# Kernel tuning notes

Hardware: AMD Instinct MI355X
Metric: run time of the kernel (lower is better)

The kernel has to match this reference:

```python
import jax, jax.numpy as jnp
import numpy as np

N, D, IN, HID, OUT, E = 20000, 8, 64, 128, 64, 100000
EPS = 1e-5


def _bn(h, g, b):
    # training-mode BatchNorm1d: biased batch variance, eps=1e-5
    m = h.mean(axis=0)
    v = jnp.mean((h - m) ** 2, axis=0)
    return (h - m) * jax.lax.rsqrt(v + EPS) * g + b


def setup_inputs() -> dict:
    key = jax.random.key(0)
    ks = jax.random.split(key, 12)
    x = jax.random.normal(ks[0], (N, IN), dtype=jnp.float32)
    node_ts = jax.random.uniform(ks[1], (N,), dtype=jnp.float32)
    neighbor_idx = jax.random.randint(ks[2], (N, D), 0, N, dtype=jnp.int32)
    neighbor_ts = jax.random.uniform(ks[3], (N, D), dtype=jnp.float32)
    target = jax.random.randint(ks[4], (2, E), 0, N, dtype=jnp.int32)
    neg_pairs = jax.random.randint(ks[5], (2, E), 0, N, dtype=jnp.int32)
    W1 = jax.random.normal(ks[6], (IN, HID), dtype=jnp.float32) * (1.0 / np.sqrt(IN))
    b1 = jnp.zeros((HID,), jnp.float32)
    g1 = jnp.ones((HID,), jnp.float32)
    be1 = jnp.zeros((HID,), jnp.float32)
    W2 = jax.random.normal(ks[7], (HID, OUT), dtype=jnp.float32) * (1.0 / np.sqrt(HID))
    b2 = jnp.zeros((OUT,), jnp.float32)
    g2 = jnp.ones((OUT,), jnp.float32)
    be2 = jnp.zeros((OUT,), jnp.float32)
    Wd = jax.random.normal(ks[8], (OUT, 1), dtype=jnp.float32) * (1.0 / np.sqrt(OUT))
    bd = jnp.zeros((1,), jnp.float32)
    return {"x": x, "node_ts": node_ts, "neighbor_idx": neighbor_idx,
            "neighbor_ts": neighbor_ts, "target": target, "neg_pairs": neg_pairs,
            "W1": W1, "b1": b1, "g1": g1, "be1": be1,
            "W2": W2, "b2": b2, "g2": g2, "be2": be2, "Wd": Wd, "bd": bd}


def reference(x, node_ts, neighbor_idx, neighbor_ts, target, neg_pairs,
              W1, b1, g1, be1, W2, b2, g2, be2, Wd, bd):
    n = jnp.arange(N, dtype=neighbor_idx.dtype)
    # ---- level-2 queries: every node at its own timestamp ----
    # children = D temporal-neighbor slots + self (self always valid, ts=node_ts)
    c_idx = jnp.concatenate([neighbor_idx, n[:, None]], axis=1)          # [N, D+1]
    c_ts = jnp.concatenate([neighbor_ts, node_ts[:, None]], axis=1)      # [N, D+1]
    mask2 = jnp.concatenate([neighbor_ts <= node_ts[:, None],
                             jnp.ones((N, 1), bool)], axis=1)            # [N, D+1]
    # ---- level-1 queries: each (child node, child ts) pair ----
    ci = c_idx.reshape(-1)                                               # [M]
    cts = c_ts.reshape(-1)
    gc_idx = jnp.concatenate([neighbor_idx[ci], ci[:, None]], axis=1)    # [M, D+1]
    mask1 = jnp.concatenate([neighbor_ts[ci] <= cts[:, None],
                             jnp.ones((ci.shape[0], 1), bool)], axis=1)
    # ---- layer 0: raw features of grandchildren ----
    h0 = x[gc_idx]                                                       # [M, D+1, IN]
    m1 = mask1.astype(x.dtype)
    agg1 = jnp.einsum('mk,mkf->mf', m1, h0) / m1.sum(1, keepdims=True)   # masked mean
    h1 = jax.nn.relu(_bn(agg1 @ W1 + b1, g1, be1))                       # [M, HID]
    h1 = h1.reshape(N, D + 1, HID)
    # ---- layer 2 aggregation over temporal children ----
    m2 = mask2.astype(x.dtype)
    agg2 = jnp.einsum('nk,nkf->nf', m2, h1) / m2.sum(1, keepdims=True)
    embs = jax.nn.relu(_bn(agg2 @ W2 + b2, g2, be2))                     # [N, OUT]
    # ---- HadNet link decoder + BCEWithLogits ----
    pos = (embs[target[0]] * embs[target[1]]) @ Wd + bd                  # [E, 1]
    neg = (embs[neg_pairs[0]] * embs[neg_pairs[1]]) @ Wd + bd            # [E, 1]
    preds = jnp.concatenate([pos, neg], axis=0)[:, 0]                    # [2E]
    labels = jnp.concatenate([jnp.ones((E,), x.dtype), jnp.zeros((E,), x.dtype)])
    loss = jnp.mean(jnp.maximum(preds, 0.0) - preds * labels
                    + jnp.log1p(jnp.exp(-jnp.abs(preds))))
    return loss
```

## Files before the change

### kernel.cpp

```cpp
#include <hip/hip_runtime.h>
#include <math.h>

constexpr int kN = 20000;
constexpr int kD = 8;
constexpr int kE = 100000;
constexpr int kM = kN * 9;
constexpr int kTiles1 = kM / 16;
constexpr int kTiles3 = kN / 16;
constexpr float kEps = 1e-5f;

constexpr int S_SUM1 = 0, S_SQ1 = 128, S_SUM2 = 256, S_SQ2 = 320;

constexpr size_t OFF_M     = 0;
constexpr size_t OFF_AGG1  = 23040000;
constexpr size_t OFF_AGG2  = 46080000;
constexpr size_t OFF_STATS = 51200000;
constexpr size_t OFF_PRE2  = 0;
constexpr size_t OFF_EMBS  = 5120000;
constexpr size_t OFF_EMBSW = 10240000;

typedef short short8 __attribute__((ext_vector_type(8)));
typedef float floatx4 __attribute__((ext_vector_type(4)));

__device__ __forceinline__ unsigned f2bf(float f) {
  unsigned u = __float_as_uint(f);
  u += 0x7fffu + ((u >> 16) & 1u);
  return u >> 16;
}

__global__ __launch_bounds__(256) void k0_prefix(
    const float* __restrict__ x, const int* __restrict__ nidx,
    const float* __restrict__ nts, unsigned short* __restrict__ M)
{
  int c = blockIdx.x * 4 + (threadIdx.x >> 6);
  const int lane = threadIdx.x & 63;
  c = __builtin_amdgcn_readfirstlane(c);

  float ts[8]; int id[8];
#pragma unroll
  for (int j = 0; j < kD; ++j) { ts[j] = nts[c * kD + j]; id[j] = nidx[c * kD + j]; }

#define CSWAP(A, B)                                                   \
  { float ta = ts[A], tb = ts[B]; int ia = id[A], ib = id[B];         \
    bool sw = tb < ta;                                                \
    ts[A] = sw ? tb : ta; ts[B] = sw ? ta : tb;                       \
    id[A] = sw ? ib : ia; id[B] = sw ? ia : ib; }
  CSWAP(0, 1) CSWAP(2, 3) CSWAP(0, 2) CSWAP(1, 3) CSWAP(1, 2)
  CSWAP(4, 5) CSWAP(6, 7) CSWAP(4, 6) CSWAP(5, 7) CSWAP(5, 6)
  CSWAP(0, 4) CSWAP(1, 5) CSWAP(2, 6) CSWAP(3, 7)
  CSWAP(2, 4) CSWAP(3, 5)
  CSWAP(1, 2) CSWAP(3, 4) CSWAP(5, 6)
#undef CSWAP

  float s = x[c * 64 + lane];
  unsigned short* mp = M + (size_t)c * 9 * 64 + lane;
  mp[0] = (unsigned short)f2bf(s);
#pragma unroll
  for (int r = 1; r <= kD; ++r) {
    s += x[id[r - 1] * 64 + lane];
    mp[r * 64] = (unsigned short)f2bf(s / (float)(r + 1));
  }
}

__global__ __launch_bounds__(256) void k1a_gather(
    const unsigned short* __restrict__ M, const float* __restrict__ node_ts,
    const int* __restrict__ nidx, const float* __restrict__ nts,
    unsigned short* __restrict__ agg1)
{
  const int m = blockIdx.x * 4 + (threadIdx.x >> 6);
  const int lane = threadIdx.x & 63;
  const int n = (int)((unsigned)m / 9u);
  const int slot = m - n * 9;
  int c; float t;
  if (slot < kD) { c = nidx[n * kD + slot]; t = nts[n * kD + slot]; }
  else           { c = n;                   t = node_ts[n]; }
  c = __builtin_amdgcn_readfirstlane(c);
  int rank = 0;
#pragma unroll
  for (int j = 0; j < kD; ++j) rank += (nts[c * kD + j] <= t) ? 1 : 0;
  unsigned short v = M[((size_t)c * 9 + rank) * 64 + lane];
  const int tt = m >> 4, r = m & 15, g = lane >> 3, jj = lane & 7;
  agg1[tt * 1024 + g * 128 + r * 8 + jj] = v;
}

__global__ __launch_bounds__(256, 3) void k1b_gemm1(
    const unsigned short* aggA,
    unsigned short* preLo,
    unsigned short* __restrict__ preHi,
    const float* __restrict__ W1, const float* __restrict__ b1,
    float* __restrict__ stats)
{
  __shared__ unsigned short W1T[128 * 72];
  __shared__ float redS[256][8];
  __shared__ float redQ[256][8];

  const int tid = threadIdx.x;
  const int lane = tid & 63;
  const int wave = tid >> 6;
  const int l15 = lane & 15;
  const int q = lane >> 4;

  for (int i = tid; i < 8192; i += 256) {
    int n = i >> 6, k = i & 63;
    W1T[n * 72 + k] = (unsigned short)f2bf(W1[k * 128 + n]);
  }
  __syncthreads();

  short8 bf[8][2];
#pragma unroll
  for (int c = 0; c < 8; ++c)
#pragma unroll
    for (int s = 0; s < 2; ++s)
      bf[c][s] = *(const short8*)&W1T[(c * 16 + l15) * 72 + q * 8 + s * 32];

  float b1c[8];
#pragma unroll
  for (int c = 0; c < 8; ++c) b1c[c] = b1[c * 16 + l15];

  float sum8[8], sq8[8];
#pragma unroll
  for (int c = 0; c < 8; ++c) { sum8[c] = 0.f; sq8[c] = 0.f; }

  const int gw = blockIdx.x * 4 + wave;
  const int nw = gridDim.x * 4;

  for (int t = gw; t < kTiles1; t += nw) {
    const unsigned short* ap = aggA + (size_t)t * 1024;
    short8 af0 = *(const short8*)(ap + (q)*128 + l15 * 8);
    short8 af1 = *(const short8*)(ap + (4 + q) * 128 + l15 * 8);

    floatx4 acc[8];
#pragma unroll
    for (int c = 0; c < 8; ++c) {
      acc[c] = (floatx4){0.f, 0.f, 0.f, 0.f};
      acc[c] = __builtin_amdgcn_mfma_f32_16x16x32_bf16(af0, bf[c][0], acc[c], 0, 0, 0);
      acc[c] = __builtin_amdgcn_mfma_f32_16x16x32_bf16(af1, bf[c][1], acc[c], 0, 0, 0);
    }
#pragma unroll
    for (int c = 0; c < 8; ++c) {
      int colq = (c & 3) * 16 + l15;
#pragma unroll
      for (int i = 0; i < 4; ++i) {
        float v = acc[c][i] + b1c[c];
        int row = t * 16 + q * 4 + i;
        unsigned short hv = (unsigned short)f2bf(v);
        if (c < 4) preLo[(size_t)row * 64 + colq] = hv;
        else       preHi[(size_t)row * 64 + colq] = hv;
        sum8[c] += v; sq8[c] += v * v;
      }
    }
  }

  __syncthreads();
#pragma unroll
  for (int c = 0; c < 8; ++c) { redS[tid][c] = sum8[c]; redQ[tid][c] = sq8[c]; }
  __syncthreads();
  if (tid < 128) {
    int c = tid >> 4, r15 = tid & 15;
    float s = 0.f, qq = 0.f;
#pragma unroll
    for (int w = 0; w < 4; ++w)
#pragma unroll
      for (int p = 0; p < 4; ++p) {
        int T = w * 64 + p * 16 + r15;
        s += redS[T][c]; qq += redQ[T][c];
      }
    atomicAdd(&stats[S_SUM1 + tid], s);
    atomicAdd(&stats[S_SQ1 + tid], qq);
  }
}

__global__ __launch_bounds__(256) void k3a_agg2(
    const unsigned* __restrict__ loDW, const unsigned* __restrict__ hiDW,
    const float* __restrict__ node_ts, const float* __restrict__ nts,
    const float* __restrict__ stats, const float* __restrict__ g1,
    const float* __restrict__ be1, unsigned* __restrict__ agg2dw)
{
  __shared__ float sc[128], sh[128];
  const int tid = threadIdx.x;
  if (tid < 128) {
    float mean = stats[S_SUM1 + tid] * (1.f / kM);
    float var  = stats[S_SQ1 + tid] * (1.f / kM) - mean * mean;
    float s    = g1[tid] * rsqrtf(var + kEps);
    sc[tid] = s; sh[tid] = be1[tid] - mean * s;
  }
  __syncthreads();
  const int n = blockIdx.x * 4 + (tid >> 6);
  const int L = tid & 63;
  const unsigned* base = (L < 32) ? loDW : hiDW;
  const int Lc = L & 31;
  const float sc0 = sc[2 * L], sc1 = sc[2 * L + 1];
  const float sh0 = sh[2 * L], sh1 = sh[2 * L + 1];
  const float tn = node_ts[n];
  float s0 = 0.f, s1 = 0.f, fcnt = 0.f;
#pragma unroll
  for (int slot = 0; slot < 9; ++slot) {
    float w = (slot < kD) ? ((nts[n * kD + slot] <= tn) ? 1.f : 0.f) : 1.f;
    unsigned u = base[(size_t)(n * 9 + slot) * 32 + Lc];
    float p0 = __uint_as_float(u << 16);
    float p1 = __uint_as_float(u & 0xffff0000u);
    s0 += w * fmaxf(fmaf(p0, sc0, sh0), 0.f);
    s1 += w * fmaxf(fmaf(p1, sc1, sh1), 0.f);
    fcnt += w;
  }
  float r = 1.f / fcnt;
  agg2dw[n * 64 + L] = f2bf(s0 * r) | (f2bf(s1 * r) << 16);
}

__global__ __launch_bounds__(256, 3) void k3b_gemm2(
    const unsigned short* __restrict__ agg2, const float* __restrict__ W2,
    const float* __restrict__ b2, float* __restrict__ stats,
    float* __restrict__ pre2)
{
  __shared__ unsigned short W2T[64 * 136];
  __shared__ float redS[256][4];
  __shared__ float redQ[256][4];

  const int tid = threadIdx.x;
  const int lane = tid & 63;
  const int wave = tid >> 6;
  const int l15 = lane & 15;
  const int q = lane >> 4;

  for (int i = tid; i < 8192; i += 256) {
    int n = i >> 7, k = i & 127;
    W2T[n * 136 + k] = (unsigned short)f2bf(W2[k * 64 + n]);
  }
  __syncthreads();

  short8 bfr[4][4];
#pragma unroll
  for (int c = 0; c < 4; ++c)
#pragma unroll
    for (int s = 0; s < 4; ++s)
      bfr[c][s] = *(const short8*)&W2T[(c * 16 + l15) * 136 + q * 8 + s * 32];

  float b2c[4];
#pragma unroll
  for (int c = 0; c < 4; ++c) b2c[c] = b2[c * 16 + l15];

  float sum4[4], sq4[4];
#pragma unroll
  for (int c = 0; c < 4; ++c) { sum4[c] = 0.f; sq4[c] = 0.f; }

  const int gw = blockIdx.x * 4 + wave;
  const int nw = gridDim.x * 4;

  for (int t = gw; t < kTiles3; t += nw) {
    const int r0 = t * 16;
    short8 af[4];
#pragma unroll
    for (int s = 0; s < 4; ++s)
      af[s] = *(const short8*)&agg2[(size_t)(r0 + l15) * 128 + q * 8 + s * 32];

    floatx4 acc[4];
#pragma unroll
    for (int c = 0; c < 4; ++c) {
      acc[c] = (floatx4){0.f, 0.f, 0.f, 0.f};
#pragma unroll
      for (int s = 0; s < 4; ++s)
        acc[c] = __builtin_amdgcn_mfma_f32_16x16x32_bf16(af[s], bfr[c][s], acc[c], 0, 0, 0);
    }
#pragma unroll
    for (int c = 0; c < 4; ++c) {
      int col = c * 16 + l15;
#pragma unroll
      for (int i = 0; i < 4; ++i) {
        float v = acc[c][i] + b2c[c];
        int row = r0 + q * 4 + i;
        pre2[(size_t)row * 64 + col] = v;
        sum4[c] += v; sq4[c] += v * v;
      }
    }
  }

  __syncthreads();
#pragma unroll
  for (int c = 0; c < 4; ++c) { redS[tid][c] = sum4[c]; redQ[tid][c] = sq4[c]; }
  __syncthreads();
  if (tid < 64) {
    int c = tid >> 4, r15 = tid & 15;
    float s = 0.f, qq = 0.f;
#pragma unroll
    for (int w = 0; w < 4; ++w)
#pragma unroll
      for (int p = 0; p < 4; ++p) {
        int T = w * 64 + p * 16 + r15;
        s += redS[T][c]; qq += redQ[T][c];
      }
    atomicAdd(&stats[S_SUM2 + tid], s);
    atomicAdd(&stats[S_SQ2 + tid], qq);
  }
}

__global__ __launch_bounds__(256) void k5_embs(
    const float* __restrict__ pre2, const float* __restrict__ stats,
    const float* __restrict__ g2, const float* __restrict__ be2,
    const float* __restrict__ Wd, float* __restrict__ embs,
    float* __restrict__ embsW)
{
  __shared__ float sc[64], sh[64], wd[64];
  const int tid = threadIdx.x;
  if (tid < 64) {
    float mean = stats[S_SUM2 + tid] * (1.f / kN);
    float var  = stats[S_SQ2 + tid] * (1.f / kN) - mean * mean;
    float s    = g2[tid] * rsqrtf(var + kEps);
    sc[tid] = s; sh[tid] = be2[tid] - mean * s; wd[tid] = Wd[tid];
  }
  __syncthreads();
  int idx = blockIdx.x * 256 + tid;
  int col = idx & 63;
  float e = fmaxf(fmaf(pre2[idx], sc[col], sh[col]), 0.f);
  embs[idx] = e;
  embsW[idx] = e * wd[col];
}

__global__ __launch_bounds__(256) void k6_loss(
    const float* __restrict__ embs, const float* __restrict__ embsW,
    const int* __restrict__ tgt, const int* __restrict__ neg,
    const float* __restrict__ bd, float* __restrict__ out)
{
  __shared__ float redl[256];
  const int tid = threadIdx.x;
  const int tq = tid & 15;
  const int qb = tid >> 4;
  const float bd0 = bd[0];
  float lsum = 0.f;
  const int e0 = blockIdx.x * 128 + qb * 8;
#pragma unroll
  for (int it = 0; it < 8; ++it) {
    int e = e0 + it;
    if (e < 2 * kE) {
      int i, j; float lab;
      if (e < kE) { i = tgt[e];      j = tgt[kE + e]; lab = 1.f; }
      else        { i = neg[e - kE]; j = neg[e];      lab = 0.f; }
      float4 av = *(const float4*)(embsW + (size_t)i * 64 + tq * 4);
      float4 bv = *(const float4*)(embs  + (size_t)j * 64 + tq * 4);
      float p = av.x * bv.x + av.y * bv.y + av.z * bv.z + av.w * bv.w;
      p += __shfl_xor(p, 1); p += __shfl_xor(p, 2);
      p += __shfl_xor(p, 4); p += __shfl_xor(p, 8);
      p += bd0;
      float l = fmaxf(p, 0.f) - p * lab + log1pf(expf(-fabsf(p)));
      if (tq == 0) lsum += l;
    }
  }
  redl[tid] = lsum;
  __syncthreads();
  for (int s = 128; s > 0; s >>= 1) {
    if (tid < s) redl[tid] += redl[tid + s];
    __syncthreads();
  }
  if (tid == 0) atomicAdd(out, redl[0] * (1.f / (2 * kE)));
}

extern "C" void kernel_launch(void* const* d_in, const int* in_sizes, int n_in,
                              void* d_out, int out_size, void* d_ws, size_t ws_size,
                              hipStream_t stream) {
  (void)in_sizes; (void)n_in; (void)out_size; (void)ws_size;
  const float* x       = (const float*)d_in[0];
  const float* node_ts = (const float*)d_in[1];
  const int*   nidx    = (const int*)d_in[2];
  const float* nts     = (const float*)d_in[3];
  const int*   tgt     = (const int*)d_in[4];
  const int*   neg     = (const int*)d_in[5];
  const float* W1      = (const float*)d_in[6];
  const float* b1      = (const float*)d_in[7];
  const float* g1      = (const float*)d_in[8];
  const float* be1     = (const float*)d_in[9];
  const float* W2      = (const float*)d_in[10];
  const float* b2      = (const float*)d_in[11];
  const float* g2      = (const float*)d_in[12];
  const float* be2     = (const float*)d_in[13];
  const float* Wd      = (const float*)d_in[14];
  const float* bd      = (const float*)d_in[15];

  char* ws = (char*)d_ws;
  unsigned short* Mbuf  = (unsigned short*)(ws + OFF_M);
  unsigned short* agg1  = (unsigned short*)(ws + OFF_AGG1);
  unsigned short* agg2  = (unsigned short*)(ws + OFF_AGG2);
  float* stats = (float*)(ws + OFF_STATS);
  float* pre2  = (float*)(ws + OFF_PRE2);
  float* embs  = (float*)(ws + OFF_EMBS);
  float* embsW = (float*)(ws + OFF_EMBSW);
  float* out   = (float*)d_out;

  hipMemsetAsync(stats, 0, 384 * sizeof(float), stream);
  hipMemsetAsync(out, 0, sizeof(float), stream);

  k0_prefix<<<kN / 4, 256, 0, stream>>>(x, nidx, nts, Mbuf);
  k1a_gather<<<kM / 4, 256, 0, stream>>>(Mbuf, node_ts, nidx, nts, agg1);
  k1b_gemm1<<<704, 256, 0, stream>>>(agg1, agg1, Mbuf, W1, b1, stats);
  k3a_agg2<<<kN / 4, 256, 0, stream>>>((const unsigned*)agg1, (const unsigned*)Mbuf,
                                       node_ts, nts, stats, g1, be1, (unsigned*)agg2);
  k3b_gemm2<<<160, 256, 0, stream>>>(agg2, W2, b2, stats, pre2);
  k5_embs<<<kN * 64 / 256, 256, 0, stream>>>(pre2, stats, g2, be2, Wd, embs, embsW);
  k6_loss<<<(2 * kE + 127) / 128, 256, 0, stream>>>(embs, embsW, tgt, neg, bd, out);
}
```

Measured before the change: 222.8 us.

## Replace gathered GEMM1 with count-weighted stats pass and fused recompute pipeline

```diff
diff --git a/kernel.cpp b/kernel.cpp
--- a/kernel.cpp
+++ b/kernel.cpp
@@ -6,18 +6,16 @@
 constexpr int kE = 100000;
 constexpr int kM = kN * 9;
 constexpr int kTiles1 = kM / 16;
-constexpr int kTiles3 = kN / 16;
+constexpr int kTilesN = kN / 16;
 constexpr float kEps = 1e-5f;
 
 constexpr int S_SUM1 = 0, S_SQ1 = 128, S_SUM2 = 256, S_SQ2 = 320;
 
 constexpr size_t OFF_M     = 0;
-constexpr size_t OFF_AGG1  = 23040000;
-constexpr size_t OFF_AGG2  = 46080000;
-constexpr size_t OFF_STATS = 51200000;
-constexpr size_t OFF_PRE2  = 0;
-constexpr size_t OFF_EMBS  = 5120000;
-constexpr size_t OFF_EMBSW = 10240000;
+constexpr size_t OFF_PRE2  = 23040000;
+constexpr size_t OFF_STATS = 28160000;
+constexpr size_t OFF_CNT   = OFF_STATS + 1536;
+constexpr size_t OFF_RI    = OFF_CNT + 720000;
 
 typedef short short8 __attribute__((ext_vector_type(8)));
 typedef float floatx4 __attribute__((ext_vector_type(4)));
@@ -29,8 +27,10 @@
 }
 
 __global__ __launch_bounds__(256) void k0_prefix(
-    const float* __restrict__ x, const int* __restrict__ nidx,
-    const float* __restrict__ nts, unsigned short* __restrict__ M)
+    const float* __restrict__ x, const float* __restrict__ node_ts,
+    const int* __restrict__ nidx, const float* __restrict__ nts,
+    unsigned short* __restrict__ M, int* __restrict__ rowinfo,
+    float* __restrict__ cntf)
 {
   int c = blockIdx.x * 4 + (threadIdx.x >> 6);
   const int lane = threadIdx.x & 63;
@@ -60,33 +60,24 @@
     s += x[id[r - 1] * 64 + lane];
     mp[r * 64] = (unsigned short)f2bf(s / (float)(r + 1));
   }
-}
-
-__global__ __launch_bounds__(256) void k1a_gather(
-    const unsigned short* __restrict__ M, const float* __restrict__ node_ts,
-    const int* __restrict__ nidx, const float* __restrict__ nts,
-    unsigned short* __restrict__ agg1)
-{
-  const int m = blockIdx.x * 4 + (threadIdx.x >> 6);
-  const int lane = threadIdx.x & 63;
-  const int n = (int)((unsigned)m / 9u);
-  const int slot = m - n * 9;
-  int c; float t;
-  if (slot < kD) { c = nidx[n * kD + slot]; t = nts[n * kD + slot]; }
-  else           { c = n;                   t = node_ts[n]; }
-  c = __builtin_amdgcn_readfirstlane(c);
-  int rank = 0;
-#pragma unroll
-  for (int j = 0; j < kD; ++j) rank += (nts[c * kD + j] <= t) ? 1 : 0;
-  unsigned short v = M[((size_t)c * 9 + rank) * 64 + lane];
-  const int tt = m >> 4, r = m & 15, g = lane >> 3, jj = lane & 7;
-  agg1[tt * 1024 + g * 128 + r * 8 + jj] = v;
-}
-
-__global__ __launch_bounds__(256, 3) void k1b_gemm1(
-    const unsigned short* aggA,
-    unsigned short* preLo,
-    unsigned short* __restrict__ preHi,
+
+  const int m = blockIdx.x * 256 + threadIdx.x;
+  if (m < kM) {
+    const int n = (int)((unsigned)m / 9u);
+    const int slot = m - n * 9;
+    int cc; float t;
+    if (slot < kD) { cc = nidx[n * kD + slot]; t = nts[n * kD + slot]; }
+    else           { cc = n;                   t = node_ts[n]; }
+    int rank = 0;
+#pragma unroll
+    for (int j = 0; j < kD; ++j) rank += (nts[cc * kD + j] <= t) ? 1 : 0;
+    rowinfo[m] = cc * 9 + rank;
+    atomicAdd(&cntf[cc * 9 + rank], 1.0f);
+  }
+}
+
+__global__ __launch_bounds__(256, 3) void k1_stats(
+    const unsigned short* __restrict__ M, const float* __restrict__ cntf,
     const float* __restrict__ W1, const float* __restrict__ b1,
     float* __restrict__ stats)
 {
@@ -108,113 +99,83 @@
 
   short8 bf[8][2];
 #pragma unroll
-  for (int c = 0; c < 8; ++c)
+  for (int cc = 0; cc < 8; ++cc)
 #pragma unroll
     for (int s = 0; s < 2; ++s)
-      bf[c][s] = *(const short8*)&W1T[(c * 16 + l15) * 72 + q * 8 + s * 32];
+      bf[cc][s] = *(const short8*)&W1T[(cc * 16 + l15) * 72 + q * 8 + s * 32];
 
   float b1c[8];
 #pragma unroll
-  for (int c = 0; c < 8; ++c) b1c[c] = b1[c * 16 + l15];
+  for (int cc = 0; cc < 8; ++cc) b1c[cc] = b1[cc * 16 + l15];
 
   float sum8[8], sq8[8];
 #pragma unroll
-  for (int c = 0; c < 8; ++c) { sum8[c] = 0.f; sq8[c] = 0.f; }
+  for (int cc = 0; cc < 8; ++cc) { sum8[cc] = 0.f; sq8[cc] = 0.f; }
 
   const int gw = blockIdx.x * 4 + wave;
   const int nw = gridDim.x * 4;
 
   for (int t = gw; t < kTiles1; t += nw) {
-    const unsigned short* ap = aggA + (size_t)t * 1024;
-    short8 af0 = *(const short8*)(ap + (q)*128 + l15 * 8);
-    short8 af1 = *(const short8*)(ap + (4 + q) * 128 + l15 * 8);
+    const unsigned short* mp = M + (size_t)(t * 16 + l15) * 64;
+    short8 af0 = *(const short8*)(mp + q * 8);
+    short8 af1 = *(const short8*)(mp + 32 + q * 8);
+    float c4[4];
+#pragma unroll
+    for (int i = 0; i < 4; ++i) c4[i] = cntf[t * 16 + q * 4 + i];
 
     floatx4 acc[8];
 #pragma unroll
-    for (int c = 0; c < 8; ++c) {
-      acc[c] = (floatx4){0.f, 0.f, 0.f, 0.f};
-      acc[c] = __builtin_amdgcn_mfma_f32_16x16x32_bf16(af0, bf[c][0], acc[c], 0, 0, 0);
-      acc[c] = __builtin_amdgcn_mfma_f32_16x16x32_bf16(af1, bf[c][1], acc[c], 0, 0, 0);
-    }
-#pragma unroll
-    for (int c = 0; c < 8; ++c) {
-      int colq = (c & 3) * 16 + l15;
+    for (int cc = 0; cc < 8; ++cc) {
+      acc[cc] = (floatx4){0.f, 0.f, 0.f, 0.f};
+      acc[cc] = __builtin_amdgcn_mfma_f32_16x16x32_bf16(af0, bf[cc][0], acc[cc], 0, 0, 0);
+      acc[cc] = __builtin_amdgcn_mfma_f32_16x16x32_bf16(af1, bf[cc][1], acc[cc], 0, 0, 0);
+    }
+#pragma unroll
+    for (int cc = 0; cc < 8; ++cc) {
 #pragma unroll
       for (int i = 0; i < 4; ++i) {
-        float v = acc[c][i] + b1c[c];
-        int row = t * 16 + q * 4 + i;
-        unsigned short hv = (unsigned short)f2bf(v);
-        if (c < 4) preLo[(size_t)row * 64 + colq] = hv;
-        else       preHi[(size_t)row * 64 + colq] = hv;
-        sum8[c] += v; sq8[c] += v * v;
+        float v = acc[cc][i] + b1c[cc];
+        sum8[cc] += c4[i] * v;
+        sq8[cc]  += c4[i] * v * v;
       }
     }
   }
 
   __syncthreads();
 #pragma unroll
-  for (int c = 0; c < 8; ++c) { redS[tid][c] = sum8[c]; redQ[tid][c] = sq8[c]; }
+  for (int cc = 0; cc < 8; ++cc) { redS[tid][cc] = sum8[cc]; redQ[tid][cc] = sq8[cc]; }
   __syncthreads();
   if (tid < 128) {
-    int c = tid >> 4, r15 = tid & 15;
+    int cc = tid >> 4, r15 = tid & 15;
     float s = 0.f, qq = 0.f;
 #pragma unroll
     for (int w = 0; w < 4; ++w)
 #pragma unroll
       for (int p = 0; p < 4; ++p) {
         int T = w * 64 + p * 16 + r15;
-        s += redS[T][c]; qq += redQ[T][c];
+        s += redS[T][cc]; qq += redQ[T][cc];
       }
     atomicAdd(&stats[S_SUM1 + tid], s);
     atomicAdd(&stats[S_SQ1 + tid], qq);
   }
 }
 
-__global__ __launch_bounds__(256) void k3a_agg2(
-    const unsigned* __restrict__ loDW, const unsigned* __restrict__ hiDW,
+__global__ __launch_bounds__(256, 2) void k3_fused(
+    const unsigned short* __restrict__ M, const int* __restrict__ rowinfo,
     const float* __restrict__ node_ts, const float* __restrict__ nts,
-    const float* __restrict__ stats, const float* __restrict__ g1,
-    const float* __restrict__ be1, unsigned* __restrict__ agg2dw)
-{
-  __shared__ float sc[128], sh[128];
-  const int tid = threadIdx.x;
-  if (tid < 128) {
-    float mean = stats[S_SUM1 + tid] * (1.f / kM);
-    float var  = stats[S_SQ1 + tid] * (1.f / kM) - mean * mean;
-    float s    = g1[tid] * rsqrtf(var + kEps);
-    sc[tid] = s; sh[tid] = be1[tid] - mean * s;
-  }
-  __syncthreads();
-  const int n = blockIdx.x * 4 + (tid >> 6);
-  const int L = tid & 63;
-  const unsigned* base = (L < 32) ? loDW : hiDW;
-  const int Lc = L & 31;
-  const float sc0 = sc[2 * L], sc1 = sc[2 * L + 1];
-  const float sh0 = sh[2 * L], sh1 = sh[2 * L + 1];
-  const float tn = node_ts[n];
-  float s0 = 0.f, s1 = 0.f, fcnt = 0.f;
-#pragma unroll
-  for (int slot = 0; slot < 9; ++slot) {
-    float w = (slot < kD) ? ((nts[n * kD + slot] <= tn) ? 1.f : 0.f) : 1.f;
-    unsigned u = base[(size_t)(n * 9 + slot) * 32 + Lc];
-    float p0 = __uint_as_float(u << 16);
-    float p1 = __uint_as_float(u & 0xffff0000u);
-    s0 += w * fmaxf(fmaf(p0, sc0, sh0), 0.f);
-    s1 += w * fmaxf(fmaf(p1, sc1, sh1), 0.f);
-    fcnt += w;
-  }
-  float r = 1.f / fcnt;
-  agg2dw[n * 64 + L] = f2bf(s0 * r) | (f2bf(s1 * r) << 16);
-}
-
-__global__ __launch_bounds__(256, 3) void k3b_gemm2(
-    const unsigned short* __restrict__ agg2, const float* __restrict__ W2,
-    const float* __restrict__ b2, float* __restrict__ stats,
+    const float* __restrict__ stats_in, const float* __restrict__ g1,
+    const float* __restrict__ be1, const float* __restrict__ W1,
+    const float* __restrict__ b1, const float* __restrict__ W2,
+    const float* __restrict__ b2, float* __restrict__ stats_out,
     float* __restrict__ pre2)
 {
-  __shared__ unsigned short W2T[64 * 136];
-  __shared__ float redS[256][4];
-  __shared__ float redQ[256][4];
+  __shared__ __attribute__((aligned(16))) unsigned short W1T[128 * 72];
+  __shared__ __attribute__((aligned(16))) unsigned short W2T[64 * 136];
+  __shared__ __attribute__((aligned(16))) unsigned short sm[144 * 132];
+  __shared__ __attribute__((aligned(16))) unsigned short aggT[16 * 136];
+  __shared__ float sc1[128], sh1[128];
+  __shared__ float wlds[144];
+  __shared__ float winv[16];
 
   const int tid = threadIdx.x;
   const int lane = tid & 63;
@@ -223,108 +184,153 @@
   const int q = lane >> 4;
 
   for (int i = tid; i < 8192; i += 256) {
+    int n = i >> 6, k = i & 63;
+    W1T[n * 72 + k] = (unsigned short)f2bf(W1[k * 128 + n]);
+  }
+  for (int i = tid; i < 8192; i += 256) {
     int n = i >> 7, k = i & 127;
     W2T[n * 136 + k] = (unsigned short)f2bf(W2[k * 64 + n]);
   }
-  __syncthreads();
-
-  short8 bfr[4][4];
-#pragma unroll
-  for (int c = 0; c < 4; ++c)
+  if (tid < 128) {
+    float mean = stats_in[S_SUM1 + tid] * (1.f / kM);
+    float var  = stats_in[S_SQ1 + tid] * (1.f / kM) - mean * mean;
+    float s    = g1[tid] * rsqrtf(var + kEps);
+    sc1[tid] = s; sh1[tid] = be1[tid] - mean * s;
+  }
+  __syncthreads();
+
+  short8 bf[8][2];
+  float b1c[8], scc[8], shc[8];
+#pragma unroll
+  for (int cc = 0; cc < 8; ++cc) {
+    int col = cc * 16 + l15;
+#pragma unroll
+    for (int s = 0; s < 2; ++s)
+      bf[cc][s] = *(const short8*)&W1T[col * 72 + q * 8 + s * 32];
+    b1c[cc] = b1[col]; scc[cc] = sc1[col]; shc[cc] = sh1[col];
+  }
+  short8 bfr2[4];
+#pragma unroll
+  for (int s = 0; s < 4; ++s)
+    bfr2[s] = *(const short8*)&W2T[(wave * 16 + l15) * 136 + q * 8 + s * 32];
+  const float b2w = b2[wave * 16 + l15];
+
+  float sumS = 0.f, sumQ = 0.f;
+
+  for (int tb = blockIdx.x; tb < kTilesN; tb += gridDim.x) {
+    const int node0 = tb * 16;
+    const int row0 = tb * 144;
+
+    if (tid < 144) {
+      int ln = tid / 9;
+      int slot = tid - ln * 9;
+      int nn = node0 + ln;
+      float w = 1.f;
+      if (slot < kD) w = (nts[nn * kD + slot] <= node_ts[nn]) ? 1.f : 0.f;
+      wlds[tid] = w;
+    }
+    __syncthreads();
+    if (tid < 16) {
+      float swv = 0.f;
+#pragma unroll
+      for (int r = 0; r < 9; ++r) swv += wlds[tid * 9 + r];
+      winv[tid] = 1.f / swv;
+    }
+
+    for (int tl = wave; tl < 9; tl += 4) {
+      const int ri = rowinfo[row0 + tl * 16 + l15];
+      const unsigned short* mp = M + (size_t)ri * 64;
+      short8 af0 = *(const short8*)(mp + q * 8);
+      short8 af1 = *(const short8*)(mp + 32 + q * 8);
+      floatx4 acc[8];
+#pragma unroll
+      for (int cc = 0; cc < 8; ++cc) {
+        acc[cc] = (floatx4){0.f, 0.f, 0.f, 0.f};
+        acc[cc] = __builtin_amdgcn_mfma_f32_16x16x32_bf16(af0, bf[cc][0], acc[cc], 0, 0, 0);
+        acc[cc] = __builtin_amdgcn_mfma_f32_16x16x32_bf16(af1, bf[cc][1], acc[cc], 0, 0, 0);
+      }
+#pragma unroll
+      for (int cc = 0; cc < 8; ++cc) {
+        int col = cc * 16 + l15;
+#pragma unroll
+        for (int i = 0; i < 4; ++i) {
+          float v = acc[cc][i] + b1c[cc];
+          float val = fmaxf(fmaf(v, scc[cc], shc[cc]), 0.f);
+          int rl = tl * 16 + q * 4 + i;
+          val *= wlds[rl];
+          sm[rl * 132 + col] = (unsigned short)f2bf(val);
+        }
+      }
+    }
+    __syncthreads();
+
+#pragma unroll
+    for (int k = 0; k < 4; ++k) {
+      int it = tid + k * 256;
+      int nd = it >> 6, cp = it & 63;
+      float s0 = 0.f, s1 = 0.f;
+#pragma unroll
+      for (int r = 0; r < 9; ++r) {
+        unsigned u = *(const unsigned*)&sm[(nd * 9 + r) * 132 + cp * 2];
+        s0 += __uint_as_float(u << 16);
+        s1 += __uint_as_float(u & 0xffff0000u);
+      }
+      float iv = winv[nd];
+      *(unsigned*)&aggT[nd * 136 + cp * 2] = f2bf(s0 * iv) | (f2bf(s1 * iv) << 16);
+    }
+    __syncthreads();
+
+    short8 af2[4];
 #pragma unroll
     for (int s = 0; s < 4; ++s)
-      bfr[c][s] = *(const short8*)&W2T[(c * 16 + l15) * 136 + q * 8 + s * 32];
-
-  float b2c[4];
-#pragma unroll
-  for (int c = 0; c < 4; ++c) b2c[c] = b2[c * 16 + l15];
-
-  float sum4[4], sq4[4];
-#pragma unroll
-  for (int c = 0; c < 4; ++c) { sum4[c] = 0.f; sq4[c] = 0.f; }
-
-  const int gw = blockIdx.x * 4 + wave;
-  const int nw = gridDim.x * 4;
-
-  for (int t = gw; t < kTiles3; t += nw) {
-    const int r0 = t * 16;
-    short8 af[4];
+      af2[s] = *(const short8*)&aggT[l15 * 136 + q * 8 + s * 32];
+    floatx4 acc2 = (floatx4){0.f, 0.f, 0.f, 0.f};
 #pragma unroll
     for (int s = 0; s < 4; ++s)
-      af[s] = *(const short8*)&agg2[(size_t)(r0 + l15) * 128 + q * 8 + s * 32];
-
-    floatx4 acc[4];
-#pragma unroll
-    for (int c = 0; c < 4; ++c) {
-      acc[c] = (floatx4){0.f, 0.f, 0.f, 0.f};
-#pragma unroll
-      for (int s = 0; s < 4; ++s)
-        acc[c] = __builtin_amdgcn_mfma_f32_16x16x32_bf16(af[s], bfr[c][s], acc[c], 0, 0, 0);
-    }
-#pragma unroll
-    for (int c = 0; c < 4; ++c) {
-      int col = c * 16 + l15;
-#pragma unroll
-      for (int i = 0; i < 4; ++i) {
-        float v = acc[c][i] + b2c[c];
-        int row = r0 + q * 4 + i;
-        pre2[(size_t)row * 64 + col] = v;
-        sum4[c] += v; sq4[c] += v * v;
-      }
-    }
-  }
-
-  __syncthreads();
-#pragma unroll
-  for (int c = 0; c < 4; ++c) { redS[tid][c] = sum4[c]; redQ[tid][c] = sq4[c]; }
-  __syncthreads();
-  if (tid < 64) {
-    int c = tid >> 4, r15 = tid & 15;
-    float s = 0.f, qq = 0.f;
-#pragma unroll
-    for (int w = 0; w < 4; ++w)
-#pragma unroll
-      for (int p = 0; p < 4; ++p) {
-        int T = w * 64 + p * 16 + r15;
-        s += redS[T][c]; qq += redQ[T][c];
-      }
-    atomicAdd(&stats[S_SUM2 + tid], s);
-    atomicAdd(&stats[S_SQ2 + tid], qq);
-  }
-}
-
-__global__ __launch_bounds__(256) void k5_embs(
+      acc2 = __builtin_amdgcn_mfma_f32_16x16x32_bf16(af2[s], bfr2[s], acc2, 0, 0, 0);
+#pragma unroll
+    for (int i = 0; i < 4; ++i) {
+      float v = acc2[i] + b2w;
+      int nrow = node0 + q * 4 + i;
+      pre2[(size_t)nrow * 64 + wave * 16 + l15] = v;
+      sumS += v; sumQ += v * v;
+    }
+  }
+
+  sumS += __shfl_xor(sumS, 16); sumS += __shfl_xor(sumS, 32);
+  sumQ += __shfl_xor(sumQ, 16); sumQ += __shfl_xor(sumQ, 32);
+  if (lane < 16) {
+    atomicAdd(&stats_out[S_SUM2 + wave * 16 + lane], sumS);
+    atomicAdd(&stats_out[S_SQ2 + wave * 16 + lane], sumQ);
+  }
+}
+
+__global__ __launch_bounds__(256) void k6_loss(
     const float* __restrict__ pre2, const float* __restrict__ stats,
     const float* __restrict__ g2, const float* __restrict__ be2,
-    const float* __restrict__ Wd, float* __restrict__ embs,
-    float* __restrict__ embsW)
+    const float* __restrict__ Wd, const int* __restrict__ tgt,
+    const int* __restrict__ neg, const float* __restrict__ bd,
+    float* __restrict__ out)
 {
-  __shared__ float sc[64], sh[64], wd[64];
+  __shared__ float scl[64], shl[64], wdl[64];
+  __shared__ float redl[256];
   const int tid = threadIdx.x;
   if (tid < 64) {
     float mean = stats[S_SUM2 + tid] * (1.f / kN);
     float var  = stats[S_SQ2 + tid] * (1.f / kN) - mean * mean;
     float s    = g2[tid] * rsqrtf(var + kEps);
-    sc[tid] = s; sh[tid] = be2[tid] - mean * s; wd[tid] = Wd[tid];
-  }
-  __syncthreads();
-  int idx = blockIdx.x * 256 + tid;
-  int col = idx & 63;
-  float e = fmaxf(fmaf(pre2[idx], sc[col], sh[col]), 0.f);
-  embs[idx] = e;
-  embsW[idx] = e * wd[col];
-}
-
-__global__ __launch_bounds__(256) void k6_loss(
-    const float* __restrict__ embs, const float* __restrict__ embsW,
-    const int* __restrict__ tgt, const int* __restrict__ neg,
-    const float* __restrict__ bd, float* __restrict__ out)
-{
-  __shared__ float redl[256];
-  const int tid = threadIdx.x;
+    scl[tid] = s; shl[tid] = be2[tid] - mean * s; wdl[tid] = Wd[tid];
+  }
+  __syncthreads();
+
   const int tq = tid & 15;
   const int qb = tid >> 4;
+  const int c0 = tq * 4;
+  const float4 sc4 = {scl[c0], scl[c0 + 1], scl[c0 + 2], scl[c0 + 3]};
+  const float4 sh4 = {shl[c0], shl[c0 + 1], shl[c0 + 2], shl[c0 + 3]};
+  const float4 wd4 = {wdl[c0], wdl[c0 + 1], wdl[c0 + 2], wdl[c0 + 3]};
   const float bd0 = bd[0];
+
   float lsum = 0.f;
   const int e0 = blockIdx.x * 128 + qb * 8;
 #pragma unroll
@@ -334,9 +340,17 @@
       int i, j; float lab;
       if (e < kE) { i = tgt[e];      j = tgt[kE + e]; lab = 1.f; }
       else        { i = neg[e - kE]; j = neg[e];      lab = 0.f; }
-      float4 av = *(const float4*)(embsW + (size_t)i * 64 + tq * 4);
-      float4 bv = *(const float4*)(embs  + (size_t)j * 64 + tq * 4);
-      float p = av.x * bv.x + av.y * bv.y + av.z * bv.z + av.w * bv.w;
+      float4 a = *(const float4*)(pre2 + (size_t)i * 64 + c0);
+      float4 b = *(const float4*)(pre2 + (size_t)j * 64 + c0);
+      float eix = fmaxf(fmaf(a.x, sc4.x, sh4.x), 0.f) * wd4.x;
+      float eiy = fmaxf(fmaf(a.y, sc4.y, sh4.y), 0.f) * wd4.y;
+      float eiz = fmaxf(fmaf(a.z, sc4.z, sh4.z), 0.f) * wd4.z;
+      float eiw = fmaxf(fmaf(a.w, sc4.w, sh4.w), 0.f) * wd4.w;
+      float ejx = fmaxf(fmaf(b.x, sc4.x, sh4.x), 0.f);
+      float ejy = fmaxf(fmaf(b.y, sc4.y, sh4.y), 0.f);
+      float ejz = fmaxf(fmaf(b.z, sc4.z, sh4.z), 0.f);
+      float ejw = fmaxf(fmaf(b.w, sc4.w, sh4.w), 0.f);
+      float p = eix * ejx + eiy * ejy + eiz * ejz + eiw * ejw;
       p += __shfl_xor(p, 1); p += __shfl_xor(p, 2);
       p += __shfl_xor(p, 4); p += __shfl_xor(p, 8);
       p += bd0;
@@ -375,24 +389,20 @@
   const float* bd      = (const float*)d_in[15];
 
   char* ws = (char*)d_ws;
-  unsigned short* Mbuf  = (unsigned short*)(ws + OFF_M);
-  unsigned short* agg1  = (unsigned short*)(ws + OFF_AGG1);
-  unsigned short* agg2  = (unsigned short*)(ws + OFF_AGG2);
+  unsigned short* Mbuf = (unsigned short*)(ws + OFF_M);
+  float* pre2  = (float*)(ws + OFF_PRE2);
   float* stats = (float*)(ws + OFF_STATS);
-  float* pre2  = (float*)(ws + OFF_PRE2);
-  float* embs  = (float*)(ws + OFF_EMBS);
-  float* embsW = (float*)(ws + OFF_EMBSW);
+  float* cntf  = (float*)(ws + OFF_CNT);
+  int*   rinfo = (int*)(ws + OFF_RI);
   float* out   = (float*)d_out;
 
-  hipMemsetAsync(stats, 0, 384 * sizeof(float), stream);
+  hipMemsetAsync(stats, 0, 1536 + 720000, stream);
   hipMemsetAsync(out, 0, sizeof(float), stream);
 
-  k0_prefix<<<kN / 4, 256, 0, stream>>>(x, nidx, nts, Mbuf);
-  k1a_gather<<<kM / 4, 256, 0, stream>>>(Mbuf, node_ts, nidx, nts, agg1);
-  k1b_gemm1<<<704, 256, 0, stream>>>(agg1, agg1, Mbuf, W1, b1, stats);
-  k3a_agg2<<<kN / 4, 256, 0, stream>>>((const unsigned*)agg1, (const unsigned*)Mbuf,
-                                       node_ts, nts, stats, g1, be1, (unsigned*)agg2);
-  k3b_gemm2<<<160, 256, 0, stream>>>(agg2, W2, b2, stats, pre2);
-  k5_embs<<<kN * 64 / 256, 256, 0, stream>>>(pre2, stats, g2, be2, Wd, embs, embsW);
-  k6_loss<<<(2 * kE + 127) / 128, 256, 0, stream>>>(embs, embsW, tgt, neg, bd, out);
-}
+  k0_prefix<<<kN / 4, 256, 0, stream>>>(x, node_ts, nidx, nts, Mbuf, rinfo, cntf);
+  k1_stats<<<704, 256, 0, stream>>>(Mbuf, cntf, W1, b1, stats);
+  k3_fused<<<512, 256, 0, stream>>>(Mbuf, rinfo, node_ts, nts, stats, g1, be1,
+                                    W1, b1, W2, b2, stats, pre2);
+  k6_loss<<<(2 * kE + 127) / 128, 256, 0, stream>>>(pre2, stats, g2, be2, Wd,
+                                                    tgt, neg, bd, out);
+}
```

Result: faster. 207.1 us (-7.0%).
